# Kernel optimization log

Hardware: AMD Instinct MI355X
Metric: run time of the kernel (lower is better)

## Reference

```python
import jax, jax.numpy as jnp
import numpy as np

N = 100000      # nodes
E = 1600000     # edges
G = 128         # graphs in batch
F_IN = 128
HID = 32
NCLS = 10


def _gcn_conv(x, src, dst, norm, W, b):
    # x: [N, Fin] -> [N, Fout]; src/dst/norm include self-loops: [E+N]
    h = x @ W                                   # dense transform first (Fout=32 < Fin)
    msg = h[src] * norm[:, None]                # gather + edge normalization
    out = jax.ops.segment_sum(msg, dst, num_segments=N)  # scatter-add
    return out + b


def setup_inputs() -> dict:
    key = jax.random.key(0)
    ks = jax.random.split(key, 10)
    x = jax.random.normal(ks[0], (N, F_IN), dtype=jnp.float32)
    edge_index = jax.random.randint(ks[1], (2, E), 0, N, dtype=jnp.int64)
    batch = jnp.sort(jax.random.randint(ks[2], (N,), 0, G, dtype=jnp.int64))
    s = 1.0 / np.sqrt(F_IN)
    W0 = jax.random.normal(ks[3], (F_IN, HID), dtype=jnp.float32) * s
    b0 = jnp.zeros((HID,), dtype=jnp.float32)
    sh = 1.0 / np.sqrt(HID)
    W1 = jax.random.normal(ks[4], (HID, HID), dtype=jnp.float32) * sh
    b1 = jnp.zeros((HID,), dtype=jnp.float32)
    W2 = jax.random.normal(ks[5], (HID, HID), dtype=jnp.float32) * sh
    b2 = jnp.zeros((HID,), dtype=jnp.float32)
    Wl = jax.random.normal(ks[6], (HID, NCLS), dtype=jnp.float32) * sh
    bl = jnp.zeros((NCLS,), dtype=jnp.float32)
    return {"x": x, "edge_index": edge_index, "batch": batch,
            "W0": W0, "b0": b0, "W1": W1, "b1": b1,
            "W2": W2, "b2": b2, "Wl": Wl, "bl": bl}


def reference(x, edge_index, batch, W0, b0, W1, b1, W2, b2, Wl, bl):
    # Self-loop augmented edge list (PyG GCNConv default: add_self_loops=True)
    loop = jnp.arange(N, dtype=edge_index.dtype)
    src = jnp.concatenate([edge_index[0], loop])    # [E+N]
    dst = jnp.concatenate([edge_index[1], loop])
    # Symmetric normalization D^{-1/2} (A+I) D^{-1/2}
    deg = jax.ops.segment_sum(jnp.ones_like(src, dtype=x.dtype), dst, num_segments=N)
    dinv = jax.lax.rsqrt(deg)                       # deg >= 1 thanks to self-loops
    norm = dinv[src] * dinv[dst]                    # [E+N]

    h = x
    for (W, b) in ((W0, b0), (W1, b1), (W2, b2)):
        h = jax.nn.relu(_gcn_conv(h, src, dst, norm, W, b))

    # global mean pool over graphs
    sums = jax.ops.segment_sum(h, batch, num_segments=G)           # [G, HID]
    cnts = jax.ops.segment_sum(jnp.ones((N,), h.dtype), batch, num_segments=G)
    pooled = sums / jnp.maximum(cnts, 1.0)[:, None]

    logits = jax.nn.relu(pooled @ Wl + bl)
    return jax.nn.log_softmax(logits, axis=1)
```

## Files before the change

kernel.cpp:

```cpp
#include <hip/hip_runtime.h>
#include <hip/hip_bf16.h>

#define NN 100000
#define NE 1600000
#define NG 128
#define FIN 128
#define HID 32
#define NCLS 10

#define EG4 (NE / 4)

#define NSL 32
#define GPS (EG4 / NSL)
#define RS 8
#define SUBN (NN / RS)
#define CSRGRID (RS * NSL)
#define CSR_T 1024

#define PAD 16
#define NEP (NE + NN * PAD + 64)

#define SCAN_B 1024
#define NB ((NN + SCAN_B - 1) / SCAN_B)

#define POOL_CHUNK 512
#define POOL_SEG 16
#define POOL_GSPAN 32
#define POOL_GRID ((NN + POOL_CHUNK - 1) / POOL_CHUNK)

#define G0_NODES 64
#define G0_GRID ((NN + G0_NODES - 1) / G0_NODES)
#define XPAD 136

#define AGG_GRID (NN / 4)

typedef int int4v __attribute__((ext_vector_type(4)));
typedef __attribute__((ext_vector_type(8))) short short8;
typedef __attribute__((ext_vector_type(4))) float f32x4;

__device__ inline unsigned short f2bf(float f) {
    unsigned int u = __float_as_uint(f);
    unsigned int r = u + 0x7FFFu + ((u >> 16) & 1u);
    return (unsigned short)(r >> 16);
}
__device__ inline float bf2f(unsigned short v) {
    return __uint_as_float(((unsigned int)v) << 16);
}

__global__ void k_init(float* __restrict__ gsum, float* __restrict__ gcnt,
                       unsigned short* __restrict__ tzero) {
    int i = blockIdx.x * blockDim.x + threadIdx.x;
    if (i < NG * HID) gsum[i] = 0.f;
    if (i < NG) gcnt[i] = 0.f;
    if (i < HID) tzero[i] = 0;
}

__global__ __launch_bounds__(CSR_T) void k_hist3(const int* __restrict__ dst,
                                                 unsigned char* __restrict__ partial) {
    const int r = blockIdx.x & (RS - 1);
    const int s = blockIdx.x >> 3;
    const int node0 = r * SUBN;
    __shared__ int lcnt[SUBN];
    for (int k = threadIdx.x; k < SUBN; k += CSR_T) lcnt[k] = 0;
    __syncthreads();
    const int g1 = (s + 1) * GPS;
    for (int g = s * GPS + threadIdx.x; g < g1; g += CSR_T) {
        const int4v d = *((const int4v*)dst + g);
        unsigned k;
        k = (unsigned)(d.x - node0); if (k < SUBN) atomicAdd(&lcnt[k], 1);
        k = (unsigned)(d.y - node0); if (k < SUBN) atomicAdd(&lcnt[k], 1);
        k = (unsigned)(d.z - node0); if (k < SUBN) atomicAdd(&lcnt[k], 1);
        k = (unsigned)(d.w - node0); if (k < SUBN) atomicAdd(&lcnt[k], 1);
    }
    __syncthreads();
    for (int k = threadIdx.x; k < SUBN; k += CSR_T)
        partial[s * NN + node0 + k] = (unsigned char)lcnt[k];
}

__global__ void k_scanA(unsigned char* __restrict__ partial, int* __restrict__ row_ptr,
                        int* __restrict__ bsum, float* __restrict__ dinv,
                        int* __restrict__ deg) {
    __shared__ int lds[SCAN_B];
    int i = blockIdx.x * SCAN_B + threadIdx.x;
    int pv = 0;
    if (i < NN) {
        int run = 0;
#pragma unroll
        for (int s = 0; s < NSL; s++) {
            int c = partial[s * NN + i];
            partial[s * NN + i] = (unsigned char)run;
            run += c;
        }
        deg[i] = run;
        dinv[i] = rsqrtf((float)run + 1.0f);
        pv = (run + PAD - 1) & ~(PAD - 1);
    }
    lds[threadIdx.x] = pv;
    __syncthreads();
    int val = pv;
    for (int off = 1; off < SCAN_B; off <<= 1) {
        int u = 0;
        if ((int)threadIdx.x >= off) u = lds[threadIdx.x - off];
        __syncthreads();
        if ((int)threadIdx.x >= off) { val += u; lds[threadIdx.x] = val; }
        __syncthreads();
    }
    if (i < NN) row_ptr[i] = val - pv;
    if (threadIdx.x == SCAN_B - 1) bsum[blockIdx.x] = val;
}

__global__ void k_scanB(int* __restrict__ bsum) {
    __shared__ int lds[128];
    int t = threadIdx.x;
    int v = (t < NB) ? bsum[t] : 0;
    lds[t] = v;
    __syncthreads();
    int val = v;
    for (int off = 1; off < 128; off <<= 1) {
        int u = 0;
        if (t >= off) u = lds[t - off];
        __syncthreads();
        if (t >= off) { val += u; lds[t] = val; }
        __syncthreads();
    }
    if (t < NB) bsum[t] = val - v;
}

__global__ void k_scanC(int* __restrict__ row_ptr, const int* __restrict__ bsum,
                        const int* __restrict__ deg, int* __restrict__ csr_src) {
    int i = blockIdx.x * SCAN_B + threadIdx.x;
    if (i < NN) {
        int r = row_ptr[i] + bsum[blockIdx.x];
        row_ptr[i] = r;
        int d = deg[i];
        int pd = (d + PAD - 1) & ~(PAD - 1);
        if (i == NN - 1) row_ptr[NN] = r + pd;
        for (int j = r + d; j < r + pd; j++) csr_src[j] = NN;
    }
}

__global__ __launch_bounds__(CSR_T) void k_scat3(const int* __restrict__ src,
                                                 const int* __restrict__ dst,
                                                 const int* __restrict__ row_ptr,
                                                 const unsigned char* __restrict__ pref,
                                                 int* __restrict__ csr_src) {
    const int r = blockIdx.x & (RS - 1);
    const int s = blockIdx.x >> 3;
    const int node0 = r * SUBN;
    __shared__ int lcur[SUBN];
    for (int k = threadIdx.x; k < SUBN; k += CSR_T)
        lcur[k] = row_ptr[node0 + k] + (int)pref[s * NN + node0 + k];
    __syncthreads();
    const int g1 = (s + 1) * GPS;
    for (int g = s * GPS + threadIdx.x; g < g1; g += CSR_T) {
        const int4v d = *((const int4v*)dst + g);
        const int4v sx = *((const int4v*)src + g);
        unsigned k;
        k = (unsigned)(d.x - node0); if (k < SUBN) { int p = atomicAdd(&lcur[k], 1); csr_src[p] = sx.x; }
        k = (unsigned)(d.y - node0); if (k < SUBN) { int p = atomicAdd(&lcur[k], 1); csr_src[p] = sx.y; }
        k = (unsigned)(d.z - node0); if (k < SUBN) { int p = atomicAdd(&lcur[k], 1); csr_src[p] = sx.z; }
        k = (unsigned)(d.w - node0); if (k < SUBN) { int p = atomicAdd(&lcur[k], 1); csr_src[p] = sx.w; }
    }
}

__global__ void k_gemm0(const float* __restrict__ x, const float* __restrict__ W,
                        const float* __restrict__ dinv, unsigned short* __restrict__ t) {
    __shared__ __align__(16) unsigned short x_lds[G0_NODES][XPAD];
    __shared__ __align__(16) unsigned short wt_lds[HID][XPAD];
    const int tid = threadIdx.x;
    const int node0 = blockIdx.x * G0_NODES;

#pragma unroll
    for (int r = 0; r < 8; r++) {
        int q = tid + 256 * r;
        int row = q >> 5;
        int c4 = q & 31;
        float4 xv = {0.f, 0.f, 0.f, 0.f};
        int node = node0 + row;
        if (node < NN) xv = ((const float4*)(x + (size_t)node * FIN))[c4];
        ushort4 b;
        b.x = f2bf(xv.x); b.y = f2bf(xv.y); b.z = f2bf(xv.z); b.w = f2bf(xv.w);
        *(ushort4*)&x_lds[row][c4 * 4] = b;
    }
#pragma unroll
    for (int r = 0; r < 16; r++) {
        int q = tid + 256 * r;
        int k = q >> 5, n = q & 31;
        wt_lds[n][k] = f2bf(W[q]);
    }
    __syncthreads();

    const int w = tid >> 6;
    const int lane = tid & 63;
    const int row = lane & 15;
    const int kg = lane >> 4;
    const int w16 = w * 16;

    f32x4 acc0 = {0.f, 0.f, 0.f, 0.f};
    f32x4 acc1 = {0.f, 0.f, 0.f, 0.f};
#pragma unroll
    for (int s = 0; s < 4; s++) {
        short8 a  = *(const short8*)&x_lds[w16 + row][s * 32 + kg * 8];
        short8 b0 = *(const short8*)&wt_lds[row][s * 32 + kg * 8];
        short8 b1 = *(const short8*)&wt_lds[16 + row][s * 32 + kg * 8];
        acc0 = __builtin_amdgcn_mfma_f32_16x16x32_bf16(a, b0, acc0, 0, 0, 0);
        acc1 = __builtin_amdgcn_mfma_f32_16x16x32_bf16(a, b1, acc1, 0, 0, 0);
    }

    const int f = lane & 15;
#pragma unroll
    for (int j = 0; j < 4; j++) {
        int node = node0 + w16 + kg * 4 + j;
        if (node < NN) {
            float di = dinv[node];
            t[(size_t)node * HID + f]      = f2bf(acc0[j] * di);
            t[(size_t)node * HID + 16 + f] = f2bf(acc1[j] * di);
        }
    }
}

__global__ void k_gemmh(const unsigned short* __restrict__ h, const float* __restrict__ W,
                        const float* __restrict__ dinv, unsigned short* __restrict__ t) {
    __shared__ float Ws[HID * HID];
    for (int j = threadIdx.x; j < HID * HID; j += 256) Ws[j] = W[j];
    __syncthreads();
    int gid = blockIdx.x * 256 + threadIdx.x;
    int i = gid >> 5, f = gid & 31;
    if (i >= NN) return;
    const short8* hr = (const short8*)(h + (size_t)i * HID);
    float acc = 0.f;
#pragma unroll
    for (int q = 0; q < 4; q++) {
        short8 hv = hr[q];
#pragma unroll
        for (int j = 0; j < 8; j++) {
            int k = q * 8 + j;
            acc = fmaf(bf2f((unsigned short)hv[j]), Ws[k * HID + f], acc);
        }
    }
    t[(size_t)i * HID + f] = f2bf(acc * dinv[i]);
}

__global__ __launch_bounds__(256, 8) void k_agg(const unsigned short* __restrict__ t,
                                                const int* __restrict__ row_ptr,
                                                const int* __restrict__ csr_src,
                                                const float* __restrict__ dinv,
                                                const float* __restrict__ b,
                                                unsigned short* __restrict__ hout) {
    const int wid = (blockIdx.x * 256 + threadIdx.x) >> 6;
    if (wid >= NN) return;
    const int lane = threadIdx.x & 63;
    const int fp = lane & 15;
    const int sub = lane >> 4;
    const int beg = row_ptr[wid], end = row_ptr[wid + 1];
    const unsigned* tw = (const unsigned*)t;

    float accLo = 0.f, accHi = 0.f;
    if (sub == 0) {
        unsigned u = tw[(size_t)wid * 16 + fp];
        accLo = __uint_as_float(u << 16);
        accHi = __uint_as_float(u & 0xFFFF0000u);
    }

    int e = beg;
    int4v ia;
    if (e < end) ia = *(const int4v*)(csr_src + e + sub * 4);
    while (e < end) {
        const int4v ca = ia;
        const int en = e + 16;
        if (en < end) ia = *(const int4v*)(csr_src + en + sub * 4);
        unsigned u0 = tw[(size_t)ca.x * 16 + fp];
        unsigned u1 = tw[(size_t)ca.y * 16 + fp];
        unsigned u2 = tw[(size_t)ca.z * 16 + fp];
        unsigned u3 = tw[(size_t)ca.w * 16 + fp];
        accLo += __uint_as_float(u0 << 16);
        accHi += __uint_as_float(u0 & 0xFFFF0000u);
        accLo += __uint_as_float(u1 << 16);
        accHi += __uint_as_float(u1 & 0xFFFF0000u);
        accLo += __uint_as_float(u2 << 16);
        accHi += __uint_as_float(u2 & 0xFFFF0000u);
        accLo += __uint_as_float(u3 << 16);
        accHi += __uint_as_float(u3 & 0xFFFF0000u);
        e = en;
    }
    accLo += __shfl_xor(accLo, 16, 64);
    accHi += __shfl_xor(accHi, 16, 64);
    accLo += __shfl_xor(accLo, 32, 64);
    accHi += __shfl_xor(accHi, 32, 64);
    if (sub == 0) {
        float di = dinv[wid];
        float rLo = fmaxf(fmaf(accLo, di, b[2 * fp]), 0.f);
        float rHi = fmaxf(fmaf(accHi, di, b[2 * fp + 1]), 0.f);
        unsigned out = (unsigned)f2bf(rLo) | ((unsigned)f2bf(rHi) << 16);
        ((unsigned*)hout)[(size_t)wid * 16 + fp] = out;
    }
}

__global__ void k_pool2(const unsigned short* __restrict__ h, const int* __restrict__ batch,
                        float* __restrict__ gsum, float* __restrict__ gcnt) {
    __shared__ float lacc[POOL_GSPAN][HID];
    __shared__ float lcnt[POOL_GSPAN];
    __shared__ int s_gmin;
    const int chunk_start = blockIdx.x * POOL_CHUNK;

    for (int j = threadIdx.x; j < POOL_GSPAN * HID; j += 256) ((float*)lacc)[j] = 0.f;
    if (threadIdx.x < POOL_GSPAN) lcnt[threadIdx.x] = 0.f;
    if (threadIdx.x == 0) {
        int cs = chunk_start < NN ? chunk_start : NN - 1;
        s_gmin = batch[cs];
    }
    __syncthreads();
    const int gmin = s_gmin;

    const int seg = threadIdx.x >> 3;
    const int l = (threadIdx.x & 7) * 4;
    const int i0 = chunk_start + seg * POOL_SEG;

    float4 acc = {0.f, 0.f, 0.f, 0.f};
    float cnt = 0.f;
    int cur_g = -1;

    for (int k = 0; k < POOL_SEG; k++) {
        int i = i0 + k;
        if (i >= NN) break;
        int g = batch[i];
        if (g != cur_g) {
            if (cur_g >= 0) {
                int bin = cur_g - gmin;
                if (bin >= 0 && bin < POOL_GSPAN) {
                    atomicAdd(&lacc[bin][l + 0], acc.x);
                    atomicAdd(&lacc[bin][l + 1], acc.y);
                    atomicAdd(&lacc[bin][l + 2], acc.z);
                    atomicAdd(&lacc[bin][l + 3], acc.w);
                    if (l == 0) atomicAdd(&lcnt[bin], cnt);
                } else {
                    atomicAdd(&gsum[cur_g * HID + l + 0], acc.x);
                    atomicAdd(&gsum[cur_g * HID + l + 1], acc.y);
                    atomicAdd(&gsum[cur_g * HID + l + 2], acc.z);
                    atomicAdd(&gsum[cur_g * HID + l + 3], acc.w);
                    if (l == 0) atomicAdd(&gcnt[cur_g], cnt);
                }
            }
            cur_g = g;
            acc.x = acc.y = acc.z = acc.w = 0.f;
            cnt = 0.f;
        }
        const ushort4 v = *(const ushort4*)&h[(size_t)i * HID + l];
        acc.x += bf2f(v.x); acc.y += bf2f(v.y);
        acc.z += bf2f(v.z); acc.w += bf2f(v.w);
        cnt += 1.f;
    }
    if (cur_g >= 0) {
        int bin = cur_g - gmin;
        if (bin >= 0 && bin < POOL_GSPAN) {
            atomicAdd(&lacc[bin][l + 0], acc.x);
            atomicAdd(&lacc[bin][l + 1], acc.y);
            atomicAdd(&lacc[bin][l + 2], acc.z);
            atomicAdd(&lacc[bin][l + 3], acc.w);
            if (l == 0) atomicAdd(&lcnt[bin], cnt);
        } else {
            atomicAdd(&gsum[cur_g * HID + l + 0], acc.x);
            atomicAdd(&gsum[cur_g * HID + l + 1], acc.y);
            atomicAdd(&gsum[cur_g * HID + l + 2], acc.z);
            atomicAdd(&gsum[cur_g * HID + l + 3], acc.w);
            if (l == 0) atomicAdd(&gcnt[cur_g], cnt);
        }
    }
    __syncthreads();

    for (int j = threadIdx.x; j < POOL_GSPAN * HID; j += 256) {
        int bin = j / HID, f = j % HID;
        int g = gmin + bin;
        float v = lacc[bin][f];
        if (g < NG && v != 0.f) atomicAdd(&gsum[g * HID + f], v);
    }
    if (threadIdx.x < POOL_GSPAN) {
        int g = gmin + threadIdx.x;
        float c = lcnt[threadIdx.x];
        if (g < NG && c != 0.f) atomicAdd(&gcnt[g], c);
    }
}

__global__ void k_classify(const float* __restrict__ gsum, const float* __restrict__ gcnt,
                           const float* __restrict__ Wl, const float* __restrict__ bl,
                           float* __restrict__ out) {
    __shared__ float w[HID * NCLS];
    __shared__ float bb[NCLS];
    int t = threadIdx.x;
    for (int j = t; j < HID * NCLS; j += blockDim.x) w[j] = Wl[j];
    if (t < NCLS) bb[t] = bl[t];
    __syncthreads();
    if (t >= NG) return;
    float c = gcnt[t];
    c = c > 1.f ? c : 1.f;
    float p[HID];
#pragma unroll
    for (int k = 0; k < HID; k++) p[k] = gsum[t * HID + k] / c;
    float lg[NCLS];
    float m = -1e30f;
#pragma unroll
    for (int c2 = 0; c2 < NCLS; c2++) {
        float a = bb[c2];
#pragma unroll
        for (int k = 0; k < HID; k++) a = fmaf(p[k], w[k * NCLS + c2], a);
        a = a > 0.f ? a : 0.f;
        lg[c2] = a;
        m = fmaxf(m, a);
    }
    float s = 0.f;
#pragma unroll
    for (int c2 = 0; c2 < NCLS; c2++) s += expf(lg[c2] - m);
    float ls = logf(s);
#pragma unroll
    for (int c2 = 0; c2 < NCLS; c2++) out[t * NCLS + c2] = lg[c2] - m - ls;
}

extern "C" void kernel_launch(void* const* d_in, const int* in_sizes, int n_in,
                              void* d_out, int out_size, void* d_ws, size_t ws_size,
                              hipStream_t stream) {
    const float* x  = (const float*)d_in[0];
    const int* ei   = (const int*)d_in[1];
    const int* batch = (const int*)d_in[2];
    const float* W0 = (const float*)d_in[3];
    const float* b0 = (const float*)d_in[4];
    const float* W1 = (const float*)d_in[5];
    const float* b1 = (const float*)d_in[6];
    const float* W2 = (const float*)d_in[7];
    const float* b2 = (const float*)d_in[8];
    const float* Wl = (const float*)d_in[9];
    const float* bl = (const float*)d_in[10];
    float* out = (float*)d_out;

    const int* esrc = ei;
    const int* edst = ei + NE;

    char* ws = (char*)d_ws;
    size_t off = 0;
    auto alloc = [&](size_t bytes) -> void* {
        void* p = ws + off;
        off = (off + bytes + 511) & ~(size_t)511;
        return p;
    };
    int*   row_ptr = (int*)alloc((NN + 1) * sizeof(int));
    float* dinv    = (float*)alloc(NN * sizeof(float));
    int*   deg     = (int*)alloc(NN * sizeof(int));
    int*   bsum    = (int*)alloc(256 * sizeof(int));
    int*   csr_src = (int*)alloc((size_t)NEP * sizeof(int));
    unsigned short* tbuf = (unsigned short*)alloc((size_t)(NN + 1) * HID * sizeof(unsigned short));
    unsigned short* hA   = (unsigned short*)alloc((size_t)NN * HID * sizeof(unsigned short));
    unsigned short* hB   = (unsigned short*)alloc((size_t)NN * HID * sizeof(unsigned short));
    float* gsum    = (float*)alloc(NG * HID * sizeof(float));
    float* gcnt    = (float*)alloc(NG * sizeof(float));
    (void)ws_size; (void)in_sizes; (void)n_in; (void)out_size;

    unsigned char* partial = (unsigned char*)tbuf;
    unsigned short* tzero = tbuf + (size_t)NN * HID;

    k_init<<<17, 256, 0, stream>>>(gsum, gcnt, tzero);
    k_hist3<<<CSRGRID, CSR_T, 0, stream>>>(edst, partial);
    k_scanA<<<NB, SCAN_B, 0, stream>>>(partial, row_ptr, bsum, dinv, deg);
    k_scanB<<<1, 128, 0, stream>>>(bsum);
    k_scanC<<<NB, SCAN_B, 0, stream>>>(row_ptr, bsum, deg, csr_src);
    k_scat3<<<CSRGRID, CSR_T, 0, stream>>>(esrc, edst, row_ptr, partial, csr_src);

    const int gemm_grid = (NN * HID + 255) / 256;

    k_gemm0<<<G0_GRID, 256, 0, stream>>>(x, W0, dinv, tbuf);
    k_agg<<<AGG_GRID, 256, 0, stream>>>(tbuf, row_ptr, csr_src, dinv, b0, hA);
    k_gemmh<<<gemm_grid, 256, 0, stream>>>(hA, W1, dinv, tbuf);
    k_agg<<<AGG_GRID, 256, 0, stream>>>(tbuf, row_ptr, csr_src, dinv, b1, hB);
    k_gemmh<<<gemm_grid, 256, 0, stream>>>(hB, W2, dinv, tbuf);
    k_agg<<<AGG_GRID, 256, 0, stream>>>(tbuf, row_ptr, csr_src, dinv, b2, hA);

    k_pool2<<<POOL_GRID, 256, 0, stream>>>(hA, batch, gsum, gcnt);
    k_classify<<<1, 128, 0, stream>>>(gsum, gcnt, Wl, bl, out);
}
```

Baseline: 224.3 us.

## Fuse the hidden-layer dense transform into the aggregation kernel epilogue

Removes the separate k_gemmh launches by having each aggregation wavefront apply bias+ReLU and then multiply by the next layer's 32x32 weight (held in LDS) via shuffles, writing the pre-scaled transformed features directly. This drops two kernel launches and a full write+read of the hidden activations per layer. The hA buffer gains a zero sentinel row so it can act as the gather source. The cost is an extra LDS weight load per block and shuffle/FMA work in the epilogue. The early return for out-of-range waves is removed, which is safe only because the grid divides NN exactly.

```diff
diff --git a/kernel.cpp b/kernel.cpp
--- a/kernel.cpp
+++ b/kernel.cpp
@@ -48,11 +48,12 @@
 }
 
 __global__ void k_init(float* __restrict__ gsum, float* __restrict__ gcnt,
-                       unsigned short* __restrict__ tzero) {
+                       unsigned short* __restrict__ tzero,
+                       unsigned short* __restrict__ hzero) {
     int i = blockIdx.x * blockDim.x + threadIdx.x;
     if (i < NG * HID) gsum[i] = 0.f;
     if (i < NG) gcnt[i] = 0.f;
-    if (i < HID) tzero[i] = 0;
+    if (i < HID) { tzero[i] = 0; hzero[i] = 0; }
 }
 
 __global__ __launch_bounds__(CSR_T) void k_hist3(const int* __restrict__ dst,
@@ -219,36 +220,20 @@
     }
 }
 
-__global__ void k_gemmh(const unsigned short* __restrict__ h, const float* __restrict__ W,
-                        const float* __restrict__ dinv, unsigned short* __restrict__ t) {
-    __shared__ float Ws[HID * HID];
-    for (int j = threadIdx.x; j < HID * HID; j += 256) Ws[j] = W[j];
-    __syncthreads();
-    int gid = blockIdx.x * 256 + threadIdx.x;
-    int i = gid >> 5, f = gid & 31;
-    if (i >= NN) return;
-    const short8* hr = (const short8*)(h + (size_t)i * HID);
-    float acc = 0.f;
-#pragma unroll
-    for (int q = 0; q < 4; q++) {
-        short8 hv = hr[q];
-#pragma unroll
-        for (int j = 0; j < 8; j++) {
-            int k = q * 8 + j;
-            acc = fmaf(bf2f((unsigned short)hv[j]), Ws[k * HID + f], acc);
-        }
-    }
-    t[(size_t)i * HID + f] = f2bf(acc * dinv[i]);
-}
-
+template <int FUSE>
 __global__ __launch_bounds__(256, 8) void k_agg(const unsigned short* __restrict__ t,
                                                 const int* __restrict__ row_ptr,
                                                 const int* __restrict__ csr_src,
                                                 const float* __restrict__ dinv,
                                                 const float* __restrict__ b,
+                                                const float* __restrict__ Wn,
                                                 unsigned short* __restrict__ hout) {
+    __shared__ float Wlds[HID * HID];
+    if (FUSE) {
+        for (int j = threadIdx.x; j < HID * HID; j += 256) Wlds[j] = Wn[j];
+        __syncthreads();
+    }
     const int wid = (blockIdx.x * 256 + threadIdx.x) >> 6;
-    if (wid >= NN) return;
     const int lane = threadIdx.x & 63;
     const int fp = lane & 15;
     const int sub = lane >> 4;
@@ -287,12 +272,32 @@
     accHi += __shfl_xor(accHi, 16, 64);
     accLo += __shfl_xor(accLo, 32, 64);
     accHi += __shfl_xor(accHi, 32, 64);
-    if (sub == 0) {
-        float di = dinv[wid];
-        float rLo = fmaxf(fmaf(accLo, di, b[2 * fp]), 0.f);
-        float rHi = fmaxf(fmaf(accHi, di, b[2 * fp + 1]), 0.f);
-        unsigned out = (unsigned)f2bf(rLo) | ((unsigned)f2bf(rHi) << 16);
-        ((unsigned*)hout)[(size_t)wid * 16 + fp] = out;
+
+    const float di = dinv[wid];
+    if (FUSE) {
+        float hLo = fmaxf(fmaf(accLo, di, b[2 * fp]), 0.f);
+        float hHi = fmaxf(fmaf(accHi, di, b[2 * fp + 1]), 0.f);
+        const int f2 = lane & 31;
+        const int hf = lane >> 5;
+        float s = 0.f;
+#pragma unroll
+        for (int k2 = 0; k2 < 8; k2++) {
+            int kk = hf * 8 + k2;
+            float hl = __shfl(hLo, kk, 64);
+            float hh = __shfl(hHi, kk, 64);
+            s = fmaf(hl, Wlds[(2 * kk) * HID + f2], s);
+            s = fmaf(hh, Wlds[(2 * kk + 1) * HID + f2], s);
+        }
+        s += __shfl_xor(s, 32, 64);
+        if (lane < 32)
+            hout[(size_t)wid * HID + f2] = f2bf(s * di);
+    } else {
+        if (sub == 0) {
+            float rLo = fmaxf(fmaf(accLo, di, b[2 * fp]), 0.f);
+            float rHi = fmaxf(fmaf(accHi, di, b[2 * fp + 1]), 0.f);
+            unsigned out = (unsigned)f2bf(rLo) | ((unsigned)f2bf(rHi) << 16);
+            ((unsigned*)hout)[(size_t)wid * 16 + fp] = out;
+        }
     }
 }
 
@@ -447,30 +452,26 @@
     int*   bsum    = (int*)alloc(256 * sizeof(int));
     int*   csr_src = (int*)alloc((size_t)NEP * sizeof(int));
     unsigned short* tbuf = (unsigned short*)alloc((size_t)(NN + 1) * HID * sizeof(unsigned short));
-    unsigned short* hA   = (unsigned short*)alloc((size_t)NN * HID * sizeof(unsigned short));
-    unsigned short* hB   = (unsigned short*)alloc((size_t)NN * HID * sizeof(unsigned short));
+    unsigned short* hA   = (unsigned short*)alloc((size_t)(NN + 1) * HID * sizeof(unsigned short));
     float* gsum    = (float*)alloc(NG * HID * sizeof(float));
     float* gcnt    = (float*)alloc(NG * sizeof(float));
     (void)ws_size; (void)in_sizes; (void)n_in; (void)out_size;
 
     unsigned char* partial = (unsigned char*)tbuf;
     unsigned short* tzero = tbuf + (size_t)NN * HID;
-
-    k_init<<<17, 256, 0, stream>>>(gsum, gcnt, tzero);
+    unsigned short* hzero = hA + (size_t)NN * HID;
+
+    k_init<<<17, 256, 0, stream>>>(gsum, gcnt, tzero, hzero);
     k_hist3<<<CSRGRID, CSR_T, 0, stream>>>(edst, partial);
     k_scanA<<<NB, SCAN_B, 0, stream>>>(partial, row_ptr, bsum, dinv, deg);
     k_scanB<<<1, 128, 0, stream>>>(bsum);
     k_scanC<<<NB, SCAN_B, 0, stream>>>(row_ptr, bsum, deg, csr_src);
     k_scat3<<<CSRGRID, CSR_T, 0, stream>>>(esrc, edst, row_ptr, partial, csr_src);
 
-    const int gemm_grid = (NN * HID + 255) / 256;
-
     k_gemm0<<<G0_GRID, 256, 0, stream>>>(x, W0, dinv, tbuf);
-    k_agg<<<AGG_GRID, 256, 0, stream>>>(tbuf, row_ptr, csr_src, dinv, b0, hA);
-    k_gemmh<<<gemm_grid, 256, 0, stream>>>(hA, W1, dinv, tbuf);
-    k_agg<<<AGG_GRID, 256, 0, stream>>>(tbuf, row_ptr, csr_src, dinv, b1, hB);
-    k_gemmh<<<gemm_grid, 256, 0, stream>>>(hB, W2, dinv, tbuf);
-    k_agg<<<AGG_GRID, 256, 0, stream>>>(tbuf, row_ptr, csr_src, dinv, b2, hA);
+    k_agg<1><<<AGG_GRID, 256, 0, stream>>>(tbuf, row_ptr, csr_src, dinv, b0, W1, hA);
+    k_agg<1><<<AGG_GRID, 256, 0, stream>>>(hA, row_ptr, csr_src, dinv, b1, W2, tbuf);
+    k_agg<0><<<AGG_GRID, 256, 0, stream>>>(tbuf, row_ptr, csr_src, dinv, b2, nullptr, hA);
 
     k_pool2<<<POOL_GRID, 256, 0, stream>>>(hA, batch, gsum, gcnt);
     k_classify<<<1, 128, 0, stream>>>(gsum, gcnt, Wl, bl, out);
```

Result: faster. 215.1 us (-4.1%).
